# Kernel tuning notes

Hardware: AMD Instinct MI355X
Metric: run time of the kernel (lower is better)

Reference implementation:

```python
import jax, jax.numpy as jnp
import numpy as np

B, D = 65536, 784          # batch, input features
H = 256                     # delegator feature (hidden) dim
L = 64                      # num_leaves (experts)
C = 10                      # num_classes


def setup_inputs() -> dict:
    key = jax.random.key(0)
    ks = jax.random.split(key, 7)
    s_in = 1.0 / np.sqrt(D)
    s_h = 1.0 / np.sqrt(H)
    return {
        "x": jax.random.normal(ks[0], (B, D), dtype=jnp.float32),
        "Wf": jax.random.normal(ks[1], (D, H), dtype=jnp.float32) * s_in,   # Node feature proj
        "bf": jnp.zeros((H,), dtype=jnp.float32),
        "Wr": jax.random.normal(ks[2], (D, L), dtype=jnp.float32) * s_in,   # Node router proj
        "br": jnp.zeros((L,), dtype=jnp.float32),
        "Wl": jax.random.normal(ks[3], (L, H, C), dtype=jnp.float32) * s_h,  # per-leaf linear
        "bl": jnp.zeros((L, C), dtype=jnp.float32),
    }


def reference(x, Wf, bf, Wr, br, Wl, bl):
    # Delegator (Node): features + routing probabilities
    features = jax.nn.relu(x @ Wf + bf)                 # [B, H]
    probs = jax.nn.softmax(x @ Wr + br, axis=1)         # [B, L]
    choices = jnp.argmax(probs, axis=1)                 # [B] top-1 leaf per sample
    # Per-sample leaf dispatch: gather each sample's leaf weights, then a
    # batched vec-mat product (memory-bound gather, low FLOP/byte).
    Wc = Wl[choices]                                    # [B, H, C]
    bc = bl[choices]                                    # [B, C]
    predictions = jnp.einsum("bh,bhc->bc", features, Wc) + bc  # [B, C]
    return predictions
```

## Files before the change

kernel.cpp:

```cpp
#include <hip/hip_runtime.h>
#include <stdint.h>

#define B_ROWS 65536
#define D_IN   784
#define H_DIM  256
#define L_LEAF 64
#define C_CLS  10
#define NSTEP  13
#define BTILE  40960
#define GAP_THRESH 0.03f

using f32x4    = __attribute__((ext_vector_type(4))) float;
using bf16x8   = __attribute__((ext_vector_type(8))) short;
using ushort8v = __attribute__((ext_vector_type(8))) unsigned short;
using ushort4v = __attribute__((ext_vector_type(4))) unsigned short;

#define O_FLAGCNT  0
#define O_CHOICES  4096
#define O_FLAGROWS (O_CHOICES + B_ROWS * 4)
#define O_WT       (O_FLAGROWS + B_ROWS * 4)
#define O_FEAT     (O_WT + NSTEP * BTILE)
#define O_WLB      (O_FEAT + (size_t)B_ROWS * H_DIM * 2)
#define WS_BASE    O_WLB
#define WS_FULL    (O_WLB + (size_t)L_LEAF * H_DIM * C_CLS * 2)

__device__ __forceinline__ unsigned short f2bf(float f) {
    union { float f; unsigned int u; } c; c.f = f;
    unsigned int u = c.u;
    return (unsigned short)((u + 0x7fffu + ((u >> 16) & 1u)) >> 16);
}
__device__ __forceinline__ float bf2f(unsigned short u) {
    union { unsigned int u; float f; } c; c.u = ((unsigned int)u) << 16;
    return c.f;
}

__device__ __forceinline__ void gload_lds16(const void* g, void* l) {
    __builtin_amdgcn_global_load_lds(
        (const __attribute__((address_space(1))) unsigned int*)g,
        (__attribute__((address_space(3))) unsigned int*)l, 16, 0, 0);
}

__global__ void k0_prep(const float* __restrict__ Wf, const float* __restrict__ Wr,
                        unsigned short* __restrict__ Wt, unsigned int* __restrict__ flagcnt) {
    if (blockIdx.x == 0 && threadIdx.x == 0) *flagcnt = 0u;
    const int ts = blockIdx.x;
    const int t  = threadIdx.x;
    #pragma unroll
    for (int i = 0; i < 10; ++i) {
        int id = i * 256 + t;
        int n  = id % 320;
        int c4 = id / 320;
        int ks = ts * 64 + ((c4 ^ (n & 7)) << 3);
        unsigned short v[8];
        #pragma unroll
        for (int j = 0; j < 8; ++j) {
            int k = ks + j;
            float f = 0.f;
            if (k < D_IN)
                f = (n < H_DIM) ? Wf[(size_t)k * H_DIM + n]
                                : Wr[(size_t)k * L_LEAF + (n - H_DIM)];
            v[j] = f2bf(f);
        }
        *(ushort8v*)((char*)Wt + (size_t)ts * BTILE + (size_t)(n * 8 + c4) * 16) = *(ushort8v*)v;
    }
}

__global__ void k0b_wl(const float* __restrict__ Wl, unsigned short* __restrict__ Wlb) {
    int i = (blockIdx.x * 256 + threadIdx.x) * 4;
    f32x4 v = *(const f32x4*)(Wl + i);
    ushort4v h; h.x = f2bf(v.x); h.y = f2bf(v.y); h.z = f2bf(v.z); h.w = f2bf(v.w);
    *(ushort4v*)(Wlb + i) = h;
}

__global__ __launch_bounds__(256, 2) void k1_gemm(
    const float* __restrict__ x, const unsigned short* __restrict__ Wt,
    const float* __restrict__ bfv, const float* __restrict__ brv,
    unsigned short* __restrict__ feat, int* __restrict__ choices,
    unsigned int* __restrict__ flagcnt, int* __restrict__ flagrows)
{
    __shared__ __align__(16) unsigned short Bl[2][320 * 64];

    const int t = threadIdx.x, w = t >> 6, l = t & 63, q = l >> 4, ic = l & 15;
    const int bm0 = blockIdx.x * 64;
    const float* xrow = x + (size_t)(bm0 + w * 16 + ic) * D_IN;

    f32x4 acc[20];
    #pragma unroll
    for (int i = 0; i < 20; ++i) acc[i] = (f32x4){0.f, 0.f, 0.f, 0.f};

    const int rb0 = ic * 64 + (((q    ) ^ (ic & 7)) << 3);
    const int rb1 = ic * 64 + (((q + 4) ^ (ic & 7)) << 3);

    #pragma unroll
    for (int i = 0; i < 10; ++i) {
        int cid = i * 256 + t;
        gload_lds16((const char*)Wt + cid * 16, (char*)&Bl[0][0] + cid * 16);
    }
    f32x4 an[4];
    #pragma unroll
    for (int kk = 0; kk < 2; ++kk) {
        int kg = kk * 32 + q * 8;
        an[2 * kk]     = *(const f32x4*)(xrow + kg);
        an[2 * kk + 1] = *(const f32x4*)(xrow + kg + 4);
    }
    __syncthreads();

    int cur = 0;
    for (int ts = 0; ts < NSTEP; ++ts) {
        if (ts + 1 < NSTEP) {
            const char* src = (const char*)Wt + (size_t)(ts + 1) * BTILE;
            char* dst = (char*)&Bl[cur ^ 1][0];
            #pragma unroll
            for (int i = 0; i < 10; ++i) {
                int cid = i * 256 + t;
                gload_lds16(src + cid * 16, dst + cid * 16);
            }
        }
        f32x4 ac0 = an[0], ac1 = an[1], ac2 = an[2], ac3 = an[3];
        if (ts + 1 < NSTEP) {
            #pragma unroll
            for (int kk = 0; kk < 2; ++kk) {
                int kg = (ts + 1) * 64 + kk * 32 + q * 8;
                if (kg + 8 <= D_IN) {
                    an[2 * kk]     = *(const f32x4*)(xrow + kg);
                    an[2 * kk + 1] = *(const f32x4*)(xrow + kg + 4);
                } else {
                    an[2 * kk]     = (f32x4){0.f, 0.f, 0.f, 0.f};
                    an[2 * kk + 1] = (f32x4){0.f, 0.f, 0.f, 0.f};
                }
            }
        }
        bf16x8 af0, af1;
        #pragma unroll
        for (int j = 0; j < 4; ++j) {
            af0[j]     = (short)f2bf(ac0[j]);
            af0[4 + j] = (short)f2bf(ac1[j]);
            af1[j]     = (short)f2bf(ac2[j]);
            af1[4 + j] = (short)f2bf(ac3[j]);
        }
        const unsigned short* Bc = &Bl[cur][0];
        #pragma unroll
        for (int nt = 0; nt < 20; ++nt) {
            bf16x8 b = *(const bf16x8*)(Bc + nt * 1024 + rb0);
            acc[nt] = __builtin_amdgcn_mfma_f32_16x16x32_bf16(af0, b, acc[nt], 0, 0, 0);
        }
        #pragma unroll
        for (int nt = 0; nt < 20; ++nt) {
            bf16x8 b = *(const bf16x8*)(Bc + nt * 1024 + rb1);
            acc[nt] = __builtin_amdgcn_mfma_f32_16x16x32_bf16(af1, b, acc[nt], 0, 0, 0);
        }
        __syncthreads();
        cur ^= 1;
    }

    #pragma unroll
    for (int nt = 0; nt < 16; ++nt) {
        int col = nt * 16 + ic;
        float bias = bfv[col];
        #pragma unroll
        for (int i = 0; i < 4; ++i) {
            int row = bm0 + w * 16 + q * 4 + i;
            float v = acc[nt][i] + bias;
            v = v > 0.f ? v : 0.f;
            feat[(size_t)row * H_DIM + col] = f2bf(v);
        }
    }
    #pragma unroll
    for (int i = 0; i < 4; ++i) {
        float m1 = -1e30f, m2 = -1e30f;
        int a1 = 0;
        #pragma unroll
        for (int nt = 16; nt < 20; ++nt) {
            int leaf = (nt - 16) * 16 + ic;
            float v = acc[nt][i] + brv[leaf];
            if (v > m1) { m2 = m1; m1 = v; a1 = leaf; }
            else if (v > m2) { m2 = v; }
        }
        #pragma unroll
        for (int s = 1; s < 16; s <<= 1) {
            float om1 = __shfl_xor(m1, s, 64);
            float om2 = __shfl_xor(m2, s, 64);
            int   oa1 = __shfl_xor(a1, s, 64);
            bool take = (om1 > m1) || (om1 == m1 && oa1 < a1);
            float nm2 = take ? fmaxf(om2, m1) : fmaxf(m2, om1);
            m1 = take ? om1 : m1;
            a1 = take ? oa1 : a1;
            m2 = nm2;
        }
        if (ic == 0) {
            int row = bm0 + w * 16 + q * 4 + i;
            choices[row] = a1;
            if (m1 - m2 < GAP_THRESH) {
                unsigned int idx = atomicAdd(flagcnt, 1u);
                flagrows[idx] = row;
            }
        }
    }
}

__global__ __launch_bounds__(256) void k2_exact(
    const float* __restrict__ x, const float* __restrict__ Wr,
    const float* __restrict__ brv, const unsigned int* __restrict__ flagcnt,
    const int* __restrict__ flagrows, int* __restrict__ choices)
{
    __shared__ float wl[64 * 64];
    __shared__ float xl[4][64];
    const unsigned int cnt = *flagcnt;
    const int t = threadIdx.x, w = t >> 6, l = t & 63;
    for (unsigned int base = blockIdx.x * 4u; base < cnt; base += gridDim.x * 4u) {
        unsigned int ri = base + w;
        int row = (ri < cnt) ? flagrows[ri] : 0;
        const float* xr = x + (size_t)row * D_IN;
        float s0 = 0.f, s1 = 0.f, s2 = 0.f, s3 = 0.f;
        for (int kt = 0; kt < NSTEP; ++kt) {
            int k0 = kt * 64;
            #pragma unroll
            for (int i = 0; i < 4; ++i) {
                int flat = i * 256 + t;
                int kk = flat >> 4, lq = (flat & 15) * 4;
                int kg = k0 + kk;
                f32x4 v = (f32x4){0.f, 0.f, 0.f, 0.f};
                if (kg < D_IN) v = *(const f32x4*)(Wr + (size_t)kg * L_LEAF + lq);
                *(f32x4*)&wl[kk * 64 + lq] = v;
            }
            xl[w][l] = (k0 + l < D_IN) ? xr[k0 + l] : 0.f;
            __syncthreads();
            #pragma unroll
            for (int kk = 0; kk < 64; kk += 4) {
                s0 = fmaf(xl[w][kk    ], wl[(kk    ) * 64 + l], s0);
                s1 = fmaf(xl[w][kk + 1], wl[(kk + 1) * 64 + l], s1);
                s2 = fmaf(xl[w][kk + 2], wl[(kk + 2) * 64 + l], s2);
                s3 = fmaf(xl[w][kk + 3], wl[(kk + 3) * 64 + l], s3);
            }
            __syncthreads();
        }
        float v = (s0 + s1) + (s2 + s3) + brv[l];
        int a = l;
        #pragma unroll
        for (int st = 1; st < 64; st <<= 1) {
            float ov = __shfl_xor(v, st, 64);
            int   oa = __shfl_xor(a, st, 64);
            if (ov > v || (ov == v && oa < a)) { v = ov; a = oa; }
        }
        if (l == 0 && ri < cnt) choices[row] = a;
    }
}

__global__ __launch_bounds__(256) void k3_leaf(
    const unsigned short* __restrict__ feat, const int* __restrict__ choices,
    const float* __restrict__ Wl, const unsigned short* __restrict__ Wlb,
    const float* __restrict__ blv, float* __restrict__ out)
{
    const int t = threadIdx.x, wv = t >> 6, l = t & 63, g = l >> 4, i = l & 15;
    const int row = blockIdx.x * 16 + wv * 4 + g;
    const int leaf = choices[row];

    ushort8v f0 = *(const ushort8v*)(feat + (size_t)row * H_DIM + i * 16);
    ushort8v f1 = *(const ushort8v*)(feat + (size_t)row * H_DIM + i * 16 + 8);
    float fv[16];
    #pragma unroll
    for (int j = 0; j < 8; ++j) { fv[j] = bf2f(f0[j]); fv[8 + j] = bf2f(f1[j]); }

    float acc[C_CLS];
    #pragma unroll
    for (int c = 0; c < C_CLS; ++c) acc[c] = 0.f;

    if (Wlb) {
        const unsigned short* wp = Wlb + ((size_t)leaf * H_DIM + i * 16) * C_CLS;
        ushort8v wreg[20];
        #pragma unroll
        for (int j = 0; j < 20; ++j) wreg[j] = *(const ushort8v*)(wp + j * 8);
        #pragma unroll
        for (int h = 0; h < 16; ++h) {
            #pragma unroll
            for (int c = 0; c < C_CLS; ++c) {
                int e = h * C_CLS + c;
                acc[c] = fmaf(fv[h], bf2f(wreg[e >> 3][e & 7]), acc[c]);
            }
        }
    } else {
        const float* wp = Wl + ((size_t)leaf * H_DIM + i * 16) * C_CLS;
        #pragma unroll
        for (int h = 0; h < 16; ++h) {
            #pragma unroll
            for (int c = 0; c < C_CLS; ++c)
                acc[c] = fmaf(fv[h], wp[h * C_CLS + c], acc[c]);
        }
    }
    #pragma unroll
    for (int st = 1; st < 16; st <<= 1) {
        #pragma unroll
        for (int c = 0; c < C_CLS; ++c) acc[c] += __shfl_xor(acc[c], st, 64);
    }
    if (i == 0) {
        #pragma unroll
        for (int c = 0; c < C_CLS; ++c)
            out[(size_t)row * C_CLS + c] = acc[c] + blv[leaf * C_CLS + c];
    }
}

extern "C" void kernel_launch(void* const* d_in, const int* in_sizes, int n_in,
                              void* d_out, int out_size, void* d_ws, size_t ws_size,
                              hipStream_t stream) {
    if (ws_size < WS_BASE) return;
    const bool use_bf = ws_size >= WS_FULL;

    const float* x   = (const float*)d_in[0];
    const float* Wf  = (const float*)d_in[1];
    const float* bfv = (const float*)d_in[2];
    const float* Wr  = (const float*)d_in[3];
    const float* brv = (const float*)d_in[4];
    const float* Wl  = (const float*)d_in[5];
    const float* blv = (const float*)d_in[6];
    float* out = (float*)d_out;

    char* ws = (char*)d_ws;
    unsigned int*   flagcnt  = (unsigned int*)(ws + O_FLAGCNT);
    int*            choices  = (int*)(ws + O_CHOICES);
    int*            flagrows = (int*)(ws + O_FLAGROWS);
    unsigned short* Wt       = (unsigned short*)(ws + O_WT);
    unsigned short* feat     = (unsigned short*)(ws + O_FEAT);
    unsigned short* Wlb      = use_bf ? (unsigned short*)(ws + O_WLB) : (unsigned short*)0;

    hipLaunchKernelGGL(k0_prep, dim3(NSTEP), dim3(256), 0, stream, Wf, Wr, Wt, flagcnt);
    if (use_bf)
        hipLaunchKernelGGL(k0b_wl, dim3(160), dim3(256), 0, stream, Wl, Wlb);
    hipLaunchKernelGGL(k1_gemm, dim3(B_ROWS / 64), dim3(256), 0, stream,
                       x, Wt, bfv, brv, feat, choices, flagcnt, flagrows);
    hipLaunchKernelGGL(k2_exact, dim3(2048), dim3(256), 0, stream,
                       x, Wr, brv, flagcnt, flagrows, choices);
    hipLaunchKernelGGL(k3_leaf, dim3(B_ROWS / 16), dim3(256), 0, stream,
                       feat, choices, Wl, Wlb, blv, out);
}
```

Measured before the change: 195.0 us.

## Split GEMM N-tiles across waves, convert activations with packed bf16 instruction

In the main GEMM kernel, each wave now covers all 64 rows of the block and owns 5 of the 20 N-tiles, instead of 16 rows across all 20 N-tiles. Each LDS B-fragment is read once per wave and reused across 4 M-tiles, so per-wave LDS traffic drops, while each wave now loads all 64 x rows itself. The fp32-to-bf16 conversion of activations now uses the hardware v_cvt_pk_bf16_f32 instruction instead of manual rounding. The weight-prep kernel is spread over 130 blocks instead of 13, and the exact-recheck kernel's grid is halved. Routing argmax now runs only in the wave that holds the router columns.

```diff
diff --git a/kernel.cpp b/kernel.cpp
--- a/kernel.cpp
+++ b/kernel.cpp
@@ -33,6 +33,11 @@
     union { unsigned int u; float f; } c; c.u = ((unsigned int)u) << 16;
     return c.f;
 }
+__device__ __forceinline__ unsigned int cvtpk(float a, float b) {
+    unsigned int r;
+    asm("v_cvt_pk_bf16_f32 %0, %1, %2" : "=v"(r) : "v"(a), "v"(b));
+    return r;
+}
 
 __device__ __forceinline__ void gload_lds16(const void* g, void* l) {
     __builtin_amdgcn_global_load_lds(
@@ -43,26 +48,23 @@
 __global__ void k0_prep(const float* __restrict__ Wf, const float* __restrict__ Wr,
                         unsigned short* __restrict__ Wt, unsigned int* __restrict__ flagcnt) {
     if (blockIdx.x == 0 && threadIdx.x == 0) *flagcnt = 0u;
-    const int ts = blockIdx.x;
-    const int t  = threadIdx.x;
-    #pragma unroll
-    for (int i = 0; i < 10; ++i) {
-        int id = i * 256 + t;
-        int n  = id % 320;
-        int c4 = id / 320;
-        int ks = ts * 64 + ((c4 ^ (n & 7)) << 3);
-        unsigned short v[8];
-        #pragma unroll
-        for (int j = 0; j < 8; ++j) {
-            int k = ks + j;
-            float f = 0.f;
-            if (k < D_IN)
-                f = (n < H_DIM) ? Wf[(size_t)k * H_DIM + n]
-                                : Wr[(size_t)k * L_LEAF + (n - H_DIM)];
-            v[j] = f2bf(f);
-        }
-        *(ushort8v*)((char*)Wt + (size_t)ts * BTILE + (size_t)(n * 8 + c4) * 16) = *(ushort8v*)v;
-    }
+    int id = blockIdx.x * 256 + threadIdx.x;
+    int ts = id / 2560;
+    int r  = id % 2560;
+    int n  = r % 320;
+    int c4 = r / 320;
+    int ks = ts * 64 + ((c4 ^ (n & 7)) << 3);
+    unsigned short v[8];
+    #pragma unroll
+    for (int j = 0; j < 8; ++j) {
+        int k = ks + j;
+        float f = 0.f;
+        if (k < D_IN)
+            f = (n < H_DIM) ? Wf[(size_t)k * H_DIM + n]
+                            : Wr[(size_t)k * L_LEAF + (n - H_DIM)];
+        v[j] = f2bf(f);
+    }
+    *(ushort8v*)((char*)Wt + (size_t)ts * BTILE + (size_t)(n * 8 + c4) * 16) = *(ushort8v*)v;
 }
 
 __global__ void k0b_wl(const float* __restrict__ Wl, unsigned short* __restrict__ Wlb) {
@@ -82,26 +84,34 @@
 
     const int t = threadIdx.x, w = t >> 6, l = t & 63, q = l >> 4, ic = l & 15;
     const int bm0 = blockIdx.x * 64;
-    const float* xrow = x + (size_t)(bm0 + w * 16 + ic) * D_IN;
-
-    f32x4 acc[20];
-    #pragma unroll
-    for (int i = 0; i < 20; ++i) acc[i] = (f32x4){0.f, 0.f, 0.f, 0.f};
+    const float* xbase = x + (size_t)(bm0 + ic) * D_IN;
+
+    f32x4 acc[4][5];
+    #pragma unroll
+    for (int a = 0; a < 4; ++a)
+        #pragma unroll
+        for (int b = 0; b < 5; ++b)
+            acc[a][b] = (f32x4){0.f, 0.f, 0.f, 0.f};
 
     const int rb0 = ic * 64 + (((q    ) ^ (ic & 7)) << 3);
     const int rb1 = ic * 64 + (((q + 4) ^ (ic & 7)) << 3);
+    const int ntb = w * 5;
 
     #pragma unroll
     for (int i = 0; i < 10; ++i) {
         int cid = i * 256 + t;
         gload_lds16((const char*)Wt + cid * 16, (char*)&Bl[0][0] + cid * 16);
     }
-    f32x4 an[4];
-    #pragma unroll
-    for (int kk = 0; kk < 2; ++kk) {
-        int kg = kk * 32 + q * 8;
-        an[2 * kk]     = *(const f32x4*)(xrow + kg);
-        an[2 * kk + 1] = *(const f32x4*)(xrow + kg + 4);
+    f32x4 an[4][4];
+    #pragma unroll
+    for (int mt = 0; mt < 4; ++mt) {
+        const float* xr = xbase + (size_t)(mt * 16) * D_IN;
+        #pragma unroll
+        for (int kk = 0; kk < 2; ++kk) {
+            int kg = kk * 32 + q * 8;
+            an[mt][2 * kk]     = *(const f32x4*)(xr + kg);
+            an[mt][2 * kk + 1] = *(const f32x4*)(xr + kg + 4);
+        }
     }
     __syncthreads();
 
@@ -116,83 +126,106 @@
                 gload_lds16(src + cid * 16, dst + cid * 16);
             }
         }
-        f32x4 ac0 = an[0], ac1 = an[1], ac2 = an[2], ac3 = an[3];
+        bf16x8 af[4][2];
+        #pragma unroll
+        for (int mt = 0; mt < 4; ++mt) {
+            #pragma unroll
+            for (int kk = 0; kk < 2; ++kk) {
+                union { unsigned int u[4]; bf16x8 v; } pk;
+                f32x4 lo = an[mt][2 * kk], hi = an[mt][2 * kk + 1];
+                pk.u[0] = cvtpk(lo.x, lo.y);
+                pk.u[1] = cvtpk(lo.z, lo.w);
+                pk.u[2] = cvtpk(hi.x, hi.y);
+                pk.u[3] = cvtpk(hi.z, hi.w);
+                af[mt][kk] = pk.v;
+            }
+        }
         if (ts + 1 < NSTEP) {
             #pragma unroll
-            for (int kk = 0; kk < 2; ++kk) {
-                int kg = (ts + 1) * 64 + kk * 32 + q * 8;
-                if (kg + 8 <= D_IN) {
-                    an[2 * kk]     = *(const f32x4*)(xrow + kg);
-                    an[2 * kk + 1] = *(const f32x4*)(xrow + kg + 4);
-                } else {
-                    an[2 * kk]     = (f32x4){0.f, 0.f, 0.f, 0.f};
-                    an[2 * kk + 1] = (f32x4){0.f, 0.f, 0.f, 0.f};
-                }
-            }
-        }
-        bf16x8 af0, af1;
-        #pragma unroll
-        for (int j = 0; j < 4; ++j) {
-            af0[j]     = (short)f2bf(ac0[j]);
-            af0[4 + j] = (short)f2bf(ac1[j]);
-            af1[j]     = (short)f2bf(ac2[j]);
-            af1[4 + j] = (short)f2bf(ac3[j]);
+            for (int mt = 0; mt < 4; ++mt) {
+                const float* xr = xbase + (size_t)(mt * 16) * D_IN;
+                #pragma unroll
+                for (int kk = 0; kk < 2; ++kk) {
+                    int kg = (ts + 1) * 64 + kk * 32 + q * 8;
+                    if (kg + 8 <= D_IN) {
+                        an[mt][2 * kk]     = *(const f32x4*)(xr + kg);
+                        an[mt][2 * kk + 1] = *(const f32x4*)(xr + kg + 4);
+                    } else {
+                        an[mt][2 * kk]     = (f32x4){0.f, 0.f, 0.f, 0.f};
+                        an[mt][2 * kk + 1] = (f32x4){0.f, 0.f, 0.f, 0.f};
+                    }
+                }
+            }
         }
         const unsigned short* Bc = &Bl[cur][0];
         #pragma unroll
-        for (int nt = 0; nt < 20; ++nt) {
-            bf16x8 b = *(const bf16x8*)(Bc + nt * 1024 + rb0);
-            acc[nt] = __builtin_amdgcn_mfma_f32_16x16x32_bf16(af0, b, acc[nt], 0, 0, 0);
-        }
-        #pragma unroll
-        for (int nt = 0; nt < 20; ++nt) {
-            bf16x8 b = *(const bf16x8*)(Bc + nt * 1024 + rb1);
-            acc[nt] = __builtin_amdgcn_mfma_f32_16x16x32_bf16(af1, b, acc[nt], 0, 0, 0);
+        for (int j = 0; j < 5; ++j) {
+            bf16x8 b = *(const bf16x8*)(Bc + (ntb + j) * 1024 + rb0);
+            #pragma unroll
+            for (int mt = 0; mt < 4; ++mt)
+                acc[mt][j] = __builtin_amdgcn_mfma_f32_16x16x32_bf16(af[mt][0], b, acc[mt][j], 0, 0, 0);
+        }
+        #pragma unroll
+        for (int j = 0; j < 5; ++j) {
+            bf16x8 b = *(const bf16x8*)(Bc + (ntb + j) * 1024 + rb1);
+            #pragma unroll
+            for (int mt = 0; mt < 4; ++mt)
+                acc[mt][j] = __builtin_amdgcn_mfma_f32_16x16x32_bf16(af[mt][1], b, acc[mt][j], 0, 0, 0);
         }
         __syncthreads();
         cur ^= 1;
     }
 
     #pragma unroll
-    for (int nt = 0; nt < 16; ++nt) {
-        int col = nt * 16 + ic;
-        float bias = bfv[col];
-        #pragma unroll
-        for (int i = 0; i < 4; ++i) {
-            int row = bm0 + w * 16 + q * 4 + i;
-            float v = acc[nt][i] + bias;
-            v = v > 0.f ? v : 0.f;
-            feat[(size_t)row * H_DIM + col] = f2bf(v);
-        }
-    }
-    #pragma unroll
-    for (int i = 0; i < 4; ++i) {
-        float m1 = -1e30f, m2 = -1e30f;
-        int a1 = 0;
-        #pragma unroll
-        for (int nt = 16; nt < 20; ++nt) {
-            int leaf = (nt - 16) * 16 + ic;
-            float v = acc[nt][i] + brv[leaf];
-            if (v > m1) { m2 = m1; m1 = v; a1 = leaf; }
-            else if (v > m2) { m2 = v; }
-        }
-        #pragma unroll
-        for (int s = 1; s < 16; s <<= 1) {
-            float om1 = __shfl_xor(m1, s, 64);
-            float om2 = __shfl_xor(m2, s, 64);
-            int   oa1 = __shfl_xor(a1, s, 64);
-            bool take = (om1 > m1) || (om1 == m1 && oa1 < a1);
-            float nm2 = take ? fmaxf(om2, m1) : fmaxf(m2, om1);
-            m1 = take ? om1 : m1;
-            a1 = take ? oa1 : a1;
-            m2 = nm2;
-        }
-        if (ic == 0) {
-            int row = bm0 + w * 16 + q * 4 + i;
-            choices[row] = a1;
-            if (m1 - m2 < GAP_THRESH) {
-                unsigned int idx = atomicAdd(flagcnt, 1u);
-                flagrows[idx] = row;
+    for (int j = 0; j < 5; ++j) {
+        int col = (ntb + j) * 16 + ic;
+        if (col < H_DIM) {
+            float bias = bfv[col];
+            #pragma unroll
+            for (int mt = 0; mt < 4; ++mt) {
+                #pragma unroll
+                for (int i = 0; i < 4; ++i) {
+                    int row = bm0 + mt * 16 + q * 4 + i;
+                    float v = acc[mt][j][i] + bias;
+                    v = v > 0.f ? v : 0.f;
+                    feat[(size_t)row * H_DIM + col] = f2bf(v);
+                }
+            }
+        }
+    }
+    if (w == 3) {
+        #pragma unroll
+        for (int mt = 0; mt < 4; ++mt) {
+            #pragma unroll
+            for (int i = 0; i < 4; ++i) {
+                float m1 = -1e30f, m2 = -1e30f;
+                int a1 = 0;
+                #pragma unroll
+                for (int j = 1; j < 5; ++j) {
+                    int leaf = (j - 1) * 16 + ic;
+                    float v = acc[mt][j][i] + brv[leaf];
+                    if (v > m1) { m2 = m1; m1 = v; a1 = leaf; }
+                    else if (v > m2) { m2 = v; }
+                }
+                #pragma unroll
+                for (int s = 1; s < 16; s <<= 1) {
+                    float om1 = __shfl_xor(m1, s, 64);
+                    float om2 = __shfl_xor(m2, s, 64);
+                    int   oa1 = __shfl_xor(a1, s, 64);
+                    bool take = (om1 > m1) || (om1 == m1 && oa1 < a1);
+                    float nm2 = take ? fmaxf(om2, m1) : fmaxf(m2, om1);
+                    m1 = take ? om1 : m1;
+                    a1 = take ? oa1 : a1;
+                    m2 = nm2;
+                }
+                if (ic == 0) {
+                    int row = bm0 + mt * 16 + q * 4 + i;
+                    choices[row] = a1;
+                    if (m1 - m2 < GAP_THRESH) {
+                        unsigned int idx = atomicAdd(flagcnt, 1u);
+                        flagrows[idx] = row;
+                    }
+                }
             }
         }
     }
@@ -322,12 +355,12 @@
     unsigned short* feat     = (unsigned short*)(ws + O_FEAT);
     unsigned short* Wlb      = use_bf ? (unsigned short*)(ws + O_WLB) : (unsigned short*)0;
 
-    hipLaunchKernelGGL(k0_prep, dim3(NSTEP), dim3(256), 0, stream, Wf, Wr, Wt, flagcnt);
+    hipLaunchKernelGGL(k0_prep, dim3(130), dim3(256), 0, stream, Wf, Wr, Wt, flagcnt);
     if (use_bf)
         hipLaunchKernelGGL(k0b_wl, dim3(160), dim3(256), 0, stream, Wl, Wlb);
     hipLaunchKernelGGL(k1_gemm, dim3(B_ROWS / 64), dim3(256), 0, stream,
                        x, Wt, bfv, brv, feat, choices, flagcnt, flagrows);
-    hipLaunchKernelGGL(k2_exact, dim3(2048), dim3(256), 0, stream,
+    hipLaunchKernelGGL(k2_exact, dim3(1024), dim3(256), 0, stream,
                        x, Wr, brv, flagcnt, flagrows, choices);
     hipLaunchKernelGGL(k3_leaf, dim3(B_ROWS / 16), dim3(256), 0, stream,
                        feat, choices, Wl, Wlb, blv, out);
```

New measurement: 206.3 us. 1.06x slower.
